# Performance work log

Hardware: AMD Instinct MI355X
Metric: run time of the kernel (lower is better)

Reference implementation:

```python
import jax, jax.numpy as jnp
import numpy as np

B, NQ, NC, D, C = 8, 1024, 4096, 256, 24  # batch, n_query, n_context, emb_dim, num_classes


def setup_inputs() -> dict:
    key = jax.random.key(0)
    ks = jax.random.split(key, 11)
    sc = 0.05  # param init scale
    return {
        "q_head": jax.random.normal(ks[0], (B, NQ, D), jnp.float32),
        "q_tail": jax.random.normal(ks[1], (B, NQ, D), jnp.float32),
        "c_head": jax.random.normal(ks[2], (B, NC, D), jnp.float32),
        "c_tail": jax.random.normal(ks[3], (B, NC, D), jnp.float32),
        "context_labels": jax.random.randint(ks[4], (B, NC), 0, C + 1),
        "mask": jnp.ones((B, NC), jnp.float32),
        "W_rel": jax.random.normal(ks[5], (2 * D, D), jnp.float32) * sc,
        "b_rel": jnp.zeros((D,), jnp.float32),
        "W_gen": jax.random.normal(ks[6], (D, C + 1), jnp.float32) * sc,
        "b_gen": jnp.zeros((C + 1,), jnp.float32),
        "W_cp": jax.random.normal(ks[7], (2 * D, 1), jnp.float32) * sc,
        "b_cp": jnp.zeros((1,), jnp.float32),
    }


def reference(q_head, q_tail, c_head, c_tail, context_labels, mask,
              W_rel, b_rel, W_gen, b_gen, W_cp, b_cp):
    def rel_emb(h, t):
        return jnp.concatenate([h, t], axis=-1) @ W_rel + b_rel

    q_emb = rel_emb(q_head, q_tail)            # [B, NQ, D]
    c_emb = rel_emb(c_head, c_tail)            # [B, NC, D]

    # generate distribution
    gen_dist = jax.nn.log_softmax(q_emb @ W_gen + b_gen, axis=-1)  # [B, NQ, C+1]

    # attention distribution (copy)
    scores = jnp.einsum('bqd,bjd->bqj', q_emb, c_emb) * mask[:, None, :]  # [B, NQ, NC]
    lsm = jax.nn.log_softmax(scores, axis=-1)
    probs = jnp.exp(lsm)
    context_vec = jnp.einsum('bqj,bjd->bqd', probs, c_emb)  # [B, NQ, D]

    # grouped logsumexp over context labels == log(sum of softmax probs per class);
    # empty classes give log(0) = -inf, matching the original -inf mask + logsumexp.
    onehot = jax.nn.one_hot(context_labels, C + 1, dtype=probs.dtype)  # [B, NC, C+1]
    copy_dist = jnp.log(jnp.einsum('bqj,bjc->bqc', probs, onehot))     # [B, NQ, C+1]

    # should-copy gate
    logits = (jnp.concatenate([q_emb, context_vec], axis=-1) @ W_cp + b_cp)[..., 0]  # [B, NQ]
    copy_prob = jax.nn.log_sigmoid(logits)[..., None]
    gen_prob = jax.nn.log_sigmoid(-logits)[..., None]

    return jnp.logaddexp(copy_prob + copy_dist, gen_prob + gen_dist)  # [B, NQ, C+1]
```

## Files before the change

### kernel.cpp

```cpp
#include <hip/hip_runtime.h>


typedef __attribute__((ext_vector_type(8))) _Float16 half8;
typedef __attribute__((ext_vector_type(4))) float floatx4;

#define WB 8
#define WNQ 1024
#define WNC 4096
#define NROWS 8192

static __device__ __forceinline__ float logsig(float x) {
    return (x >= 0.f) ? -log1pf(__expf(-x)) : x - log1pf(__expf(x));
}

union V16h { int4 v; half8 h8; _Float16 h[8]; unsigned short s[8]; uint2 u2[2]; };
union F8   { float4 v[2]; float f[8]; };
union H4   { _Float16 h[4]; uint2 u; unsigned short s[4]; };

static __device__ __forceinline__ void async_lds16(const _Float16* g, _Float16* l) {
    __builtin_amdgcn_global_load_lds(
        (const __attribute__((address_space(1))) unsigned int*)g,
        (__attribute__((address_space(3))) unsigned int*)l,
        16, 0, 0);
}

__global__ void wprep_kernel(const float* __restrict__ Wrel,
                             const float* __restrict__ Wgen,
                             const float* __restrict__ Wcp,
                             _Float16* __restrict__ WT,
                             _Float16* __restrict__ GenB)
{
    const int bx = blockIdx.x;
    if (bx < 256) {
        const int n = bx;
        for (int k = threadIdx.x; k < 512; k += 256)
            WT[(long)n * 512 + k] = (_Float16)Wrel[(long)k * 256 + n];
    } else {
        const int n = bx - 256;
        const int k = threadIdx.x;
        float v = 0.f;
        if (n < 25)       v = Wgen[(long)k * 25 + n];
        else if (n == 25) v = Wcp[k];
        GenB[(long)n * 256 + k] = (_Float16)v;
    }
}

__global__ __launch_bounds__(256, 2) void emb_kernel(
    const float* __restrict__ q_head, const float* __restrict__ q_tail,
    const float* __restrict__ c_head, const float* __restrict__ c_tail,
    const _Float16* __restrict__ WT,
    const float* __restrict__ brel,
    const _Float16* __restrict__ GenB,
    const float* __restrict__ bgen,
    _Float16* __restrict__ Qf, _Float16* __restrict__ Cf,
    _Float16* __restrict__ CfT,
    float* __restrict__ genlog)
{
    __shared__ _Float16 sA[2][2048];
    __shared__ _Float16 sO[64 * 264];

    const int tid  = threadIdx.x;
    const int lane = tid & 63;
    const int wv   = tid >> 6;
    const int l15  = lane & 15;
    const int quad = lane >> 4;
    const int n0   = wv * 64;

    const float* head; const float* tail; _Float16* Ef;
    long m0; bool isQ;
    if (blockIdx.x < 128) {
        isQ = true;  head = q_head; tail = q_tail; Ef = Qf;
        m0 = (long)blockIdx.x * 64;
    } else {
        isQ = false; head = c_head; tail = c_tail; Ef = Cf;
        m0 = (long)(blockIdx.x - 128) * 64;
    }

    const long arow = m0 + (tid >> 2);
    const int  akc  = (tid & 3) * 8;

    floatx4 acc[4][4];
#pragma unroll
    for (int a = 0; a < 4; ++a)
#pragma unroll
        for (int bq = 0; bq < 4; ++bq) acc[a][bq] = (floatx4)(0.0f);

    F8 aCur;
    aCur.v[0] = *(const float4*)(head + arow * 256 + akc);
    aCur.v[1] = *(const float4*)(head + arow * 256 + akc + 4);
    V16h wCur[4];
#pragma unroll
    for (int nt = 0; nt < 4; ++nt)
        wCur[nt].v = *(const int4*)(WT + (long)(n0 + nt * 16 + l15) * 512 + quad * 8);

    for (int ks = 0; ks < 16; ++ks) {
        {
            V16h hp;
#pragma unroll
            for (int i = 0; i < 8; ++i) hp.h[i] = (_Float16)aCur.f[i];
            *(int4*)&sA[ks & 1][tid * 8] = hp.v;
        }
        __syncthreads();

        F8 aNxt; V16h wNxt[4];
        if (ks < 15) {
            const int kg = (ks + 1) * 32;
            const float* srcb = (kg < 256) ? (head + kg) : (tail + (kg - 256));
            aNxt.v[0] = *(const float4*)(srcb + arow * 256 + akc);
            aNxt.v[1] = *(const float4*)(srcb + arow * 256 + akc + 4);
#pragma unroll
            for (int nt = 0; nt < 4; ++nt)
                wNxt[nt].v = *(const int4*)(WT + (long)(n0 + nt * 16 + l15) * 512 + kg + quad * 8);
        } else {
            aNxt = aCur;
#pragma unroll
            for (int nt = 0; nt < 4; ++nt) wNxt[nt] = wCur[nt];
        }

        V16h af[4];
#pragma unroll
        for (int mb = 0; mb < 4; ++mb)
            af[mb].v = *(const int4*)&sA[ks & 1][(mb * 16 + l15) * 32 + quad * 8];
#pragma unroll
        for (int mb = 0; mb < 4; ++mb)
#pragma unroll
            for (int nt = 0; nt < 4; ++nt)
                acc[mb][nt] = __builtin_amdgcn_mfma_f32_16x16x32_f16(af[mb].h8, wCur[nt].h8, acc[mb][nt], 0, 0, 0);

        aCur = aNxt;
#pragma unroll
        for (int nt = 0; nt < 4; ++nt) wCur[nt] = wNxt[nt];
    }

    float bias[4];
#pragma unroll
    for (int nt = 0; nt < 4; ++nt) bias[nt] = brel[n0 + nt * 16 + l15];

#pragma unroll
    for (int mb = 0; mb < 4; ++mb)
#pragma unroll
        for (int nt = 0; nt < 4; ++nt) {
            H4 hq;
#pragma unroll
            for (int r = 0; r < 4; ++r) {
                const long row = m0 + mb * 16 + quad * 4 + r;
                const _Float16 h = (_Float16)(acc[mb][nt][r] + bias[nt]);
                Ef[row * 256 + n0 + nt * 16 + l15] = h;
                hq.h[r] = h;
                if (isQ)
                    sO[(mb * 16 + quad * 4 + r) * 264 + n0 + nt * 16 + l15] = h;
            }
            if (!isQ) {
                const int n  = n0 + nt * 16 + l15;
                const int sw = (mb * 4 + quad) ^ l15;
                *(uint2*)&sO[n * 64 + sw * 4] = hq.u;
            }
        }

    __syncthreads();
    if (isQ) {
        floatx4 ga[2];
        ga[0] = (floatx4)(0.0f); ga[1] = (floatx4)(0.0f);
#pragma unroll
        for (int ks = 0; ks < 8; ++ks) {
            V16h a, b0, b1;
            a.v  = *(const int4*)&sO[(wv * 16 + l15) * 264 + ks * 32 + quad * 8];
            b0.v = *(const int4*)(GenB + (long)(l15)      * 256 + ks * 32 + quad * 8);
            b1.v = *(const int4*)(GenB + (long)(16 + l15) * 256 + ks * 32 + quad * 8);
            ga[0] = __builtin_amdgcn_mfma_f32_16x16x32_f16(a.h8, b0.h8, ga[0], 0, 0, 0);
            ga[1] = __builtin_amdgcn_mfma_f32_16x16x32_f16(a.h8, b1.h8, ga[1], 0, 0, 0);
        }
#pragma unroll
        for (int nt = 0; nt < 2; ++nt) {
            const int col = nt * 16 + l15;
            const float bb = (col < 25) ? bgen[col] : 0.f;
#pragma unroll
            for (int r = 0; r < 4; ++r)
                genlog[(m0 + wv * 16 + quad * 4 + r) * 32 + col] = ga[nt][r] + bb;
        }
    } else {
        const int bidx = (int)(m0 >> 12);
        const int jc0  = (int)(m0 & 4095);
        const int c    = tid & 7;
        const int nl   = tid >> 3;
#pragma unroll
        for (int i = 0; i < 8; ++i) {
            const int n  = nl + 32 * i;
            const int s0 = (2 * c)     ^ (n & 15);
            const int s1 = (2 * c + 1) ^ (n & 15);
            const uint2 u0 = *(const uint2*)&sO[n * 64 + s0 * 4];
            const uint2 u1 = *(const uint2*)&sO[n * 64 + s1 * 4];
            int4 out; out.x = u0.x; out.y = u0.y; out.z = u1.x; out.w = u1.y;
            *(int4*)&CfT[(long)bidx * 1048576 + (long)n * 4096 + jc0 + c * 8] = out;
        }
    }
}

__global__ __launch_bounds__(256, 2) void attn_kernel(
    const _Float16* __restrict__ qf,
    const _Float16* __restrict__ cf,
    const _Float16* __restrict__ cfT,
    const int*      __restrict__ labels,
    const float*    __restrict__ maskp,
    unsigned short* __restrict__ Oh,
    float* __restrict__ Mst,
    float* __restrict__ Lst,
    int jtiles, int nsh)
{
    __shared__ _Float16 sA[2][8192];
    __shared__ _Float16 sB[2][8192];
    __shared__ _Float16 Pw[4][16 * 40];

    const int tid  = threadIdx.x;
    const int lane = tid & 63;
    const int wv   = tid >> 6;
    const int l15  = lane & 15;
    const int quad = lane >> 4;

    const int f   = blockIdx.x;
    const int xcd = f & 7;
    const int seq = f >> 3;
    const int qt  = seq & 15;
    const int u   = seq >> 4;
    const int pr  = u * 8 + xcd;
    const int b   = pr >> nsh;
    const int sp  = pr & ((1 << nsh) - 1);
    const int q0  = qt * 64;

    V16h qfr[8];
    {
        const long qrow = (long)b * WNQ + q0 + wv * 16 + l15;
#pragma unroll
        for (int ks = 0; ks < 8; ++ks)
            qfr[ks].v = *(const int4*)(qf + qrow * 256 + ks * 32 + quad * 8);
    }

    floatx4 O[18];
#pragma unroll
    for (int i = 0; i < 18; ++i) O[i] = (floatx4)(0.0f);
    float m_run = -INFINITY;

    const int jb0 = sp * (jtiles * 32);

    auto stageTile = [&](int it, int buf) {
        const int jb = jb0 + it * 32;
        const long cbase = ((long)b * WNC + jb) * 256;
#pragma unroll
        for (int t = 0; t < 4; ++t) {
            const int idx = wv * 4 + t;
            const int ks = idx >> 1, jh = idx & 1;
            async_lds16(cf + cbase + (jh * 16 + l15) * 256 + ks * 32 + quad * 8,
                        &sA[buf][idx * 512]);
        }
        const long tbase = (long)b * 1048576 + jb;
#pragma unroll
        for (int t = 0; t < 4; ++t) {
            const int W = wv * 4 + t;
            async_lds16(cfT + tbase + (long)(W * 16 + (lane >> 2)) * 4096 + (lane & 3) * 8,
                        &sB[buf][W * 512]);
        }
    };

    stageTile(0, 0);

    for (int it = 0; it < jtiles; ++it) {
        const int cur = it & 1;
        const int jb  = jb0 + it * 32;

        __syncthreads();

        const float4 mv0 = *(const float4*)(maskp + (long)b * WNC + jb + quad * 4);
        const float4 mv1 = *(const float4*)(maskp + (long)b * WNC + jb + 16 + quad * 4);
        const int4   lb0 = *(const int4*)(labels + (long)b * WNC + jb + quad * 8);
        const int4   lb1 = *(const int4*)(labels + (long)b * WNC + jb + quad * 8 + 4);
        asm volatile("" ::: "memory");

        if (it + 1 < jtiles) stageTile(it + 1, cur ^ 1);

        floatx4 accS0 = (floatx4)(0.0f), accS1 = (floatx4)(0.0f);
        __builtin_amdgcn_s_setprio(1);
#pragma unroll
        for (int ks = 0; ks < 8; ++ks) {
            V16h a0, a1;
            a0.v = *(const int4*)&sA[cur][(ks * 2 + 0) * 512 + (quad * 16 + l15) * 8];
            a1.v = *(const int4*)&sA[cur][(ks * 2 + 1) * 512 + (quad * 16 + l15) * 8];
            accS0 = __builtin_amdgcn_mfma_f32_16x16x32_f16(a0.h8, qfr[ks].h8, accS0, 0, 0, 0);
            accS1 = __builtin_amdgcn_mfma_f32_16x16x32_f16(a1.h8, qfr[ks].h8, accS1, 0, 0, 0);
        }
        __builtin_amdgcn_s_setprio(0);
        const float* mv0p = (const float*)&mv0;
        const float* mv1p = (const float*)&mv1;
#pragma unroll
        for (int r = 0; r < 4; ++r) {
            accS0[r] *= mv0p[r];
            accS1[r] *= mv1p[r];
        }

        float v = fmaxf(fmaxf(fmaxf(accS0[0], accS0[1]), fmaxf(accS0[2], accS0[3])),
                        fmaxf(fmaxf(accS1[0], accS1[1]), fmaxf(accS1[2], accS1[3])));
        v = fmaxf(v, __shfl_xor(v, 16, 64));
        v = fmaxf(v, __shfl_xor(v, 32, 64));
        const float m_new = fmaxf(m_run, v);
        const bool upd = __any(m_new > m_run);
        const float alpha = __expf(m_run - m_new);
        float p[8];
#pragma unroll
        for (int r = 0; r < 4; ++r) {
            p[r]     = __expf(accS0[r] - m_new);
            p[4 + r] = __expf(accS1[r] - m_new);
        }
        m_run = m_new;

        if (upd) {
            float ar[4];
#pragma unroll
            for (int r = 0; r < 4; ++r) ar[r] = __shfl(alpha, quad * 4 + r, 64);
#pragma unroll
            for (int fo = 0; fo < 18; ++fo)
#pragma unroll
                for (int r = 0; r < 4; ++r) O[fo][r] *= ar[r];
        }

#pragma unroll
        for (int jf = 0; jf < 2; ++jf) {
            H4 w;
#pragma unroll
            for (int r = 0; r < 4; ++r) w.h[r] = (_Float16)p[jf * 4 + r];
            *(uint2*)&Pw[wv][l15 * 40 + jf * 16 + quad * 4] = w.u;
        }
        asm volatile("" ::: "memory");
        V16h pf;
        pf.v = *(const int4*)&Pw[wv][l15 * 40 + quad * 8];

        const int* lbp0 = (const int*)&lb0;
        const int* lbp1 = (const int*)&lb1;
        V16h oh0, oh1;
#pragma unroll
        for (int i = 0; i < 8; ++i) {
            const int lv = (i < 4) ? lbp0[i] : lbp1[i - 4];
            oh0.h[i] = (lv == l15)        ? (_Float16)1.0f : (_Float16)0.0f;
            oh1.h[i] = (lv == (l15 + 16) || l15 == 15) ? (_Float16)1.0f : (_Float16)0.0f;
        }

        __builtin_amdgcn_s_setprio(1);
#pragma unroll
        for (int dt = 0; dt < 16; ++dt) {
            V16h bfr;
            bfr.v = *(const int4*)&sB[cur][((dt * 16 + l15) * 4 + quad) * 8];
            O[dt] = __builtin_amdgcn_mfma_f32_16x16x32_f16(pf.h8, bfr.h8, O[dt], 0, 0, 0);
        }
        O[16] = __builtin_amdgcn_mfma_f32_16x16x32_f16(pf.h8, oh0.h8, O[16], 0, 0, 0);
        O[17] = __builtin_amdgcn_mfma_f32_16x16x32_f16(pf.h8, oh1.h8, O[17], 0, 0, 0);
        __builtin_amdgcn_s_setprio(0);
    }

    {
        const long base = (long)(sp * WB + b) * WNQ + q0 + wv * 16;
#pragma unroll
        for (int dt = 0; dt < 18; ++dt)
#pragma unroll
            for (int r = 0; r < 4; ++r) {
                H4 h; h.h[0] = (_Float16)O[dt][r];
                Oh[(base + quad * 4 + r) * 288 + dt * 16 + l15] = h.s[0];
            }
        if (lane < 16) Mst[base + lane] = m_run;
        if (l15 == 15) {
#pragma unroll
            for (int r = 0; r < 4; ++r)
                Lst[base + quad * 4 + r] = O[17][r];
        }
    }
}

__global__ __launch_bounds__(256) void final_kernel(
    const float* __restrict__ genlog,
    const unsigned short* __restrict__ Oh,
    const float* __restrict__ Mst,
    const float* __restrict__ Lst,
    const float* __restrict__ Wcp,
    const float* __restrict__ bcp,
    float* __restrict__ outp,
    int ns)
{
    __shared__ float gA[4][32];
    __shared__ float cdA[4][32];

    const int tid  = threadIdx.x;
    const int lane = tid & 63;
    const int wv   = tid >> 6;
    const int row  = blockIdx.x * 4 + wv;

    float ms[8];
#pragma unroll
    for (int s = 0; s < 8; ++s) ms[s] = (s < ns) ? Mst[(long)s * NROWS + row] : -INFINITY;
    float mstar = -INFINITY;
#pragma unroll
    for (int s = 0; s < 8; ++s) mstar = fmaxf(mstar, ms[s]);
    float wgt[8]; float L = 0.f;
#pragma unroll
    for (int s = 0; s < 8; ++s) {
        wgt[s] = (ms[s] == -INFINITY) ? 0.f : __expf(ms[s] - mstar);
        if (s < ns) L += Lst[(long)s * NROWS + row] * wgt[s];
    }

    const int d0 = lane * 4;
    float ctx[4] = {0.f, 0.f, 0.f, 0.f};
#pragma unroll
    for (int s = 0; s < 8; ++s) {
        if (s < ns) {
            H4 t; t.u = *(const uint2*)&Oh[((long)s * NROWS + row) * 288 + d0];
#pragma unroll
            for (int i = 0; i < 4; ++i) ctx[i] += wgt[s] * (float)t.h[i];
        }
    }

    float cls[4] = {0.f, 0.f, 0.f, 0.f};
    if (lane < 8) {
#pragma unroll
        for (int s = 0; s < 8; ++s) {
            if (s < ns) {
                H4 t; t.u = *(const uint2*)&Oh[((long)s * NROWS + row) * 288 + 256 + lane * 4];
#pragma unroll
                for (int i = 0; i < 4; ++i) cls[i] += wgt[s] * (float)t.h[i];
            }
        }
    }

    float g = (lane < 25) ? genlog[(long)row * 32 + lane] : -INFINITY;
    float mg = g;
#pragma unroll
    for (int off = 32; off >= 1; off >>= 1) mg = fmaxf(mg, __shfl_xor(mg, off, 64));
    float se = (lane < 25) ? __expf(g - mg) : 0.f;
#pragma unroll
    for (int off = 32; off >= 1; off >>= 1) se += __shfl_xor(se, off, 64);
    const float glsm = g - mg - logf(se);

    const float qgate = genlog[(long)row * 32 + 25];
    const float invL = 1.f / L;
    float part = 0.f;
#pragma unroll
    for (int i = 0; i < 4; ++i)
        part += ctx[i] * invL * Wcp[256 + d0 + i];
#pragma unroll
    for (int off = 32; off >= 1; off >>= 1) part += __shfl_xor(part, off, 64);
    const float logit = qgate + part + bcp[0];

    const float lscp  = logsig(logit);
    const float lsgen = logsig(-logit);
    const float logL  = logf(L);

    if (lane < 8) {
#pragma unroll
        for (int i = 0; i < 4; ++i)
            cdA[wv][lane * 4 + i] = (cls[i] > 0.f) ? (logf(cls[i]) - logL) : -INFINITY;
    }
    if (lane < 25) gA[wv][lane] = glsm;
    __syncthreads();

    if (lane < 25) {
        const float a  = lscp + cdA[wv][lane];
        const float bb = lsgen + gA[wv][lane];
        const float mx = fmaxf(a, bb);
        const float o  = (mx == -INFINITY) ? -INFINITY
                         : mx + log1pf(__expf(fminf(a, bb) - mx));
        outp[(long)row * 25 + lane] = o;
    }
}

extern "C" void kernel_launch(void* const* d_in, const int* in_sizes, int n_in,
                              void* d_out, int out_size, void* d_ws, size_t ws_size,
                              hipStream_t stream) {
    const float* q_head = (const float*)d_in[0];
    const float* q_tail = (const float*)d_in[1];
    const float* c_head = (const float*)d_in[2];
    const float* c_tail = (const float*)d_in[3];
    const int*   labels = (const int*)d_in[4];
    const float* maskp  = (const float*)d_in[5];
    const float* Wrel   = (const float*)d_in[6];
    const float* brel   = (const float*)d_in[7];
    const float* Wgen   = (const float*)d_in[8];
    const float* bgen   = (const float*)d_in[9];
    const float* Wcp    = (const float*)d_in[10];
    const float* bcp    = (const float*)d_in[11];

    auto need = [](long ns) -> long { return 39075840l + ns * 4784128l; };
    int ns = 4, nsh = 2;
    if ((long)ws_size < need(4)) { ns = 2; nsh = 1; }
    if ((long)ws_size < need(2)) { ns = 1; nsh = 0; }
    const int jtiles = 128 / ns;

    char* ws = (char*)d_ws;
    _Float16* Qf     = (_Float16*)(ws);
    _Float16* Cf     = (_Float16*)(ws + 4194304l);
    _Float16* CfT    = (_Float16*)(ws + 20971520l);
    _Float16* WT     = (_Float16*)(ws + 37748736l);
    _Float16* GenB   = (_Float16*)(ws + 38010880l);
    float*    genlog = (float*)   (ws + 38027264l);
    unsigned short* Oh = (unsigned short*)(ws + 39075840l);
    float*    Mst    = (float*)   (ws + 39075840l + (long)ns * 4718592l);
    float*    Lst    = Mst + (long)ns * NROWS;

    hipLaunchKernelGGL(wprep_kernel, dim3(288), dim3(256), 0, stream,
                       Wrel, Wgen, Wcp, WT, GenB);
    hipLaunchKernelGGL(emb_kernel, dim3(640), dim3(256), 0, stream,
                       q_head, q_tail, c_head, c_tail, WT, brel, GenB, bgen,
                       Qf, Cf, CfT, genlog);
    hipLaunchKernelGGL(attn_kernel, dim3(16 * 8 * ns), dim3(256), 0, stream,
                       Qf, Cf, CfT, labels, maskp, Oh, Mst, Lst, jtiles, nsh);
    hipLaunchKernelGGL(final_kernel, dim3(NROWS / 4), dim3(256), 0, stream,
                       genlog, Oh, Mst, Lst, Wcp, bcp, (float*)d_out, ns);
}
```

Before: 250.9 us.

## Process two 16-row query groups per wave to reuse context tiles

Each wave now handles 32 query rows (two 16-row groups) instead of 16, so each staged context tile in LDS feeds twice as many MFMAs. The query tile per block doubles to 128, and the split count over context rises to 8 when workspace allows, keeping the grid size unchanged. This roughly doubles accumulator registers per wave (36 floatx4 accumulators), which risks spills or lower occupancy under launch_bounds(256,2), and more splits add partial-result traffic for the final merge kernel. The sA read indexing also changes to lane*8.

```diff
diff --git a/kernel.cpp b/kernel.cpp
--- a/kernel.cpp
+++ b/kernel.cpp
@@ -209,7 +209,7 @@
 {
     __shared__ _Float16 sA[2][8192];
     __shared__ _Float16 sB[2][8192];
-    __shared__ _Float16 Pw[4][16 * 40];
+    __shared__ _Float16 Pw[4][2][16 * 40];
 
     const int tid  = threadIdx.x;
     const int lane = tid & 63;
@@ -220,25 +220,29 @@
     const int f   = blockIdx.x;
     const int xcd = f & 7;
     const int seq = f >> 3;
-    const int qt  = seq & 15;
-    const int u   = seq >> 4;
+    const int qt  = seq & 7;
+    const int u   = seq >> 3;
     const int pr  = u * 8 + xcd;
     const int b   = pr >> nsh;
     const int sp  = pr & ((1 << nsh) - 1);
-    const int q0  = qt * 64;
-
-    V16h qfr[8];
+    const int q0  = qt * 128;
+
+    V16h qfr[2][8];
     {
-        const long qrow = (long)b * WNQ + q0 + wv * 16 + l15;
-#pragma unroll
-        for (int ks = 0; ks < 8; ++ks)
-            qfr[ks].v = *(const int4*)(qf + qrow * 256 + ks * 32 + quad * 8);
-    }
-
-    floatx4 O[18];
-#pragma unroll
-    for (int i = 0; i < 18; ++i) O[i] = (floatx4)(0.0f);
-    float m_run = -INFINITY;
+        const long qrow = (long)b * WNQ + q0 + wv * 32 + l15;
+#pragma unroll
+        for (int g = 0; g < 2; ++g)
+#pragma unroll
+            for (int ks = 0; ks < 8; ++ks)
+                qfr[g][ks].v = *(const int4*)(qf + (qrow + g * 16) * 256 + ks * 32 + quad * 8);
+    }
+
+    floatx4 O[2][18];
+#pragma unroll
+    for (int g = 0; g < 2; ++g)
+#pragma unroll
+        for (int i = 0; i < 18; ++i) O[g][i] = (floatx4)(0.0f);
+    float m_run[2] = {-INFINITY, -INFINITY};
 
     const int jb0 = sp * (jtiles * 32);
 
@@ -277,60 +281,71 @@
 
         if (it + 1 < jtiles) stageTile(it + 1, cur ^ 1);
 
-        floatx4 accS0 = (floatx4)(0.0f), accS1 = (floatx4)(0.0f);
+        floatx4 accS[2][2];
+        accS[0][0] = (floatx4)(0.0f); accS[0][1] = (floatx4)(0.0f);
+        accS[1][0] = (floatx4)(0.0f); accS[1][1] = (floatx4)(0.0f);
         __builtin_amdgcn_s_setprio(1);
 #pragma unroll
         for (int ks = 0; ks < 8; ++ks) {
             V16h a0, a1;
-            a0.v = *(const int4*)&sA[cur][(ks * 2 + 0) * 512 + (quad * 16 + l15) * 8];
-            a1.v = *(const int4*)&sA[cur][(ks * 2 + 1) * 512 + (quad * 16 + l15) * 8];
-            accS0 = __builtin_amdgcn_mfma_f32_16x16x32_f16(a0.h8, qfr[ks].h8, accS0, 0, 0, 0);
-            accS1 = __builtin_amdgcn_mfma_f32_16x16x32_f16(a1.h8, qfr[ks].h8, accS1, 0, 0, 0);
+            a0.v = *(const int4*)&sA[cur][(ks * 2 + 0) * 512 + lane * 8];
+            a1.v = *(const int4*)&sA[cur][(ks * 2 + 1) * 512 + lane * 8];
+            accS[0][0] = __builtin_amdgcn_mfma_f32_16x16x32_f16(a0.h8, qfr[0][ks].h8, accS[0][0], 0, 0, 0);
+            accS[0][1] = __builtin_amdgcn_mfma_f32_16x16x32_f16(a1.h8, qfr[0][ks].h8, accS[0][1], 0, 0, 0);
+            accS[1][0] = __builtin_amdgcn_mfma_f32_16x16x32_f16(a0.h8, qfr[1][ks].h8, accS[1][0], 0, 0, 0);
+            accS[1][1] = __builtin_amdgcn_mfma_f32_16x16x32_f16(a1.h8, qfr[1][ks].h8, accS[1][1], 0, 0, 0);
         }
         __builtin_amdgcn_s_setprio(0);
+
         const float* mv0p = (const float*)&mv0;
         const float* mv1p = (const float*)&mv1;
 #pragma unroll
-        for (int r = 0; r < 4; ++r) {
-            accS0[r] *= mv0p[r];
-            accS1[r] *= mv1p[r];
-        }
-
-        float v = fmaxf(fmaxf(fmaxf(accS0[0], accS0[1]), fmaxf(accS0[2], accS0[3])),
-                        fmaxf(fmaxf(accS1[0], accS1[1]), fmaxf(accS1[2], accS1[3])));
-        v = fmaxf(v, __shfl_xor(v, 16, 64));
-        v = fmaxf(v, __shfl_xor(v, 32, 64));
-        const float m_new = fmaxf(m_run, v);
-        const bool upd = __any(m_new > m_run);
-        const float alpha = __expf(m_run - m_new);
-        float p[8];
-#pragma unroll
-        for (int r = 0; r < 4; ++r) {
-            p[r]     = __expf(accS0[r] - m_new);
-            p[4 + r] = __expf(accS1[r] - m_new);
-        }
-        m_run = m_new;
-
-        if (upd) {
-            float ar[4];
-#pragma unroll
-            for (int r = 0; r < 4; ++r) ar[r] = __shfl(alpha, quad * 4 + r, 64);
-#pragma unroll
-            for (int fo = 0; fo < 18; ++fo)
-#pragma unroll
-                for (int r = 0; r < 4; ++r) O[fo][r] *= ar[r];
-        }
-
-#pragma unroll
-        for (int jf = 0; jf < 2; ++jf) {
-            H4 w;
-#pragma unroll
-            for (int r = 0; r < 4; ++r) w.h[r] = (_Float16)p[jf * 4 + r];
-            *(uint2*)&Pw[wv][l15 * 40 + jf * 16 + quad * 4] = w.u;
+        for (int g = 0; g < 2; ++g)
+#pragma unroll
+            for (int r = 0; r < 4; ++r) {
+                accS[g][0][r] *= mv0p[r];
+                accS[g][1][r] *= mv1p[r];
+            }
+
+        V16h pf[2];
+#pragma unroll
+        for (int g = 0; g < 2; ++g) {
+            float v = fmaxf(fmaxf(fmaxf(accS[g][0][0], accS[g][0][1]), fmaxf(accS[g][0][2], accS[g][0][3])),
+                            fmaxf(fmaxf(accS[g][1][0], accS[g][1][1]), fmaxf(accS[g][1][2], accS[g][1][3])));
+            v = fmaxf(v, __shfl_xor(v, 16, 64));
+            v = fmaxf(v, __shfl_xor(v, 32, 64));
+            const float m_new = fmaxf(m_run[g], v);
+            const bool upd = __any(m_new > m_run[g]);
+            const float alpha = __expf(m_run[g] - m_new);
+            float p[8];
+#pragma unroll
+            for (int r = 0; r < 4; ++r) {
+                p[r]     = __expf(accS[g][0][r] - m_new);
+                p[4 + r] = __expf(accS[g][1][r] - m_new);
+            }
+            m_run[g] = m_new;
+
+            if (upd) {
+                float ar[4];
+#pragma unroll
+                for (int r = 0; r < 4; ++r) ar[r] = __shfl(alpha, quad * 4 + r, 64);
+#pragma unroll
+                for (int fo = 0; fo < 18; ++fo)
+#pragma unroll
+                    for (int r = 0; r < 4; ++r) O[g][fo][r] *= ar[r];
+            }
+
+#pragma unroll
+            for (int jf = 0; jf < 2; ++jf) {
+                H4 w;
+#pragma unroll
+                for (int r = 0; r < 4; ++r) w.h[r] = (_Float16)p[jf * 4 + r];
+                *(uint2*)&Pw[wv][g][l15 * 40 + jf * 16 + quad * 4] = w.u;
+            }
         }
         asm volatile("" ::: "memory");
-        V16h pf;
-        pf.v = *(const int4*)&Pw[wv][l15 * 40 + quad * 8];
+        pf[0].v = *(const int4*)&Pw[wv][0][l15 * 40 + quad * 8];
+        pf[1].v = *(const int4*)&Pw[wv][1][l15 * 40 + quad * 8];
 
         const int* lbp0 = (const int*)&lb0;
         const int* lbp1 = (const int*)&lb1;
@@ -347,27 +362,37 @@
         for (int dt = 0; dt < 16; ++dt) {
             V16h bfr;
             bfr.v = *(const int4*)&sB[cur][((dt * 16 + l15) * 4 + quad) * 8];
-            O[dt] = __builtin_amdgcn_mfma_f32_16x16x32_f16(pf.h8, bfr.h8, O[dt], 0, 0, 0);
-        }
-        O[16] = __builtin_amdgcn_mfma_f32_16x16x32_f16(pf.h8, oh0.h8, O[16], 0, 0, 0);
-        O[17] = __builtin_amdgcn_mfma_f32_16x16x32_f16(pf.h8, oh1.h8, O[17], 0, 0, 0);
+            O[0][dt] = __builtin_amdgcn_mfma_f32_16x16x32_f16(pf[0].h8, bfr.h8, O[0][dt], 0, 0, 0);
+            O[1][dt] = __builtin_amdgcn_mfma_f32_16x16x32_f16(pf[1].h8, bfr.h8, O[1][dt], 0, 0, 0);
+        }
+        O[0][16] = __builtin_amdgcn_mfma_f32_16x16x32_f16(pf[0].h8, oh0.h8, O[0][16], 0, 0, 0);
+        O[1][16] = __builtin_amdgcn_mfma_f32_16x16x32_f16(pf[1].h8, oh0.h8, O[1][16], 0, 0, 0);
+        O[0][17] = __builtin_amdgcn_mfma_f32_16x16x32_f16(pf[0].h8, oh1.h8, O[0][17], 0, 0, 0);
+        O[1][17] = __builtin_amdgcn_mfma_f32_16x16x32_f16(pf[1].h8, oh1.h8, O[1][17], 0, 0, 0);
         __builtin_amdgcn_s_setprio(0);
     }
 
     {
-        const long base = (long)(sp * WB + b) * WNQ + q0 + wv * 16;
-#pragma unroll
-        for (int dt = 0; dt < 18; ++dt)
+        const long base = (long)(sp * WB + b) * WNQ + q0 + wv * 32;
+#pragma unroll
+        for (int g = 0; g < 2; ++g)
+#pragma unroll
+            for (int dt = 0; dt < 18; ++dt)
+#pragma unroll
+                for (int r = 0; r < 4; ++r) {
+                    H4 h; h.h[0] = (_Float16)O[g][dt][r];
+                    Oh[(base + g * 16 + quad * 4 + r) * 288 + dt * 16 + l15] = h.s[0];
+                }
+        if (lane < 16) {
+            Mst[base + lane]      = m_run[0];
+            Mst[base + 16 + lane] = m_run[1];
+        }
+        if (l15 == 15) {
 #pragma unroll
             for (int r = 0; r < 4; ++r) {
-                H4 h; h.h[0] = (_Float16)O[dt][r];
-                Oh[(base + quad * 4 + r) * 288 + dt * 16 + l15] = h.s[0];
-            }
-        if (lane < 16) Mst[base + lane] = m_run;
-        if (l15 == 15) {
-#pragma unroll
-            for (int r = 0; r < 4; ++r)
-                Lst[base + quad * 4 + r] = O[17][r];
+                Lst[base + quad * 4 + r]      = O[0][17][r];
+                Lst[base + 16 + quad * 4 + r] = O[1][17][r];
+            }
         }
     }
 }
@@ -484,7 +509,8 @@
     const float* bcp    = (const float*)d_in[11];
 
     auto need = [](long ns) -> long { return 39075840l + ns * 4784128l; };
-    int ns = 4, nsh = 2;
+    int ns = 8, nsh = 3;
+    if ((long)ws_size < need(8)) { ns = 4; nsh = 2; }
     if ((long)ws_size < need(4)) { ns = 2; nsh = 1; }
     if ((long)ws_size < need(2)) { ns = 1; nsh = 0; }
     const int jtiles = 128 / ns;
@@ -505,7 +531,7 @@
     hipLaunchKernelGGL(emb_kernel, dim3(640), dim3(256), 0, stream,
                        q_head, q_tail, c_head, c_tail, WT, brel, GenB, bgen,
                        Qf, Cf, CfT, genlog);
-    hipLaunchKernelGGL(attn_kernel, dim3(16 * 8 * ns), dim3(256), 0, stream,
+    hipLaunchKernelGGL(attn_kernel, dim3(8 * 8 * ns), dim3(256), 0, stream,
                        Qf, Cf, CfT, labels, maskp, Oh, Mst, Lst, jtiles, nsh);
     hipLaunchKernelGGL(final_kernel, dim3(NROWS / 4), dim3(256), 0, stream,
                        genlog, Oh, Mst, Lst, Wcp, bcp, (float*)d_out, ns);
```

Result: slower. 390.2 us (+55.6%).
